# Kernel optimization log

Measured on AMD Instinct MI355X. Metric: run time of the kernel, lower is better.

The kernel has to match this reference:

```python
import jax, jax.numpy as jnp
import numpy as np

B, S, C = 4, 2048, 2048
D = C // 4  # head dim = 512

def setup_inputs() -> dict:
    key = jax.random.key(0)
    k1, k2, k3, k4, k5 = jax.random.split(key, 5)
    scale = 1.0 / np.sqrt(C)
    return {
        "x": jax.random.normal(k1, (B, S, C), dtype=jnp.float32),
        "Wqkv": jax.random.normal(k2, (3 * D, C), dtype=jnp.float32) * scale,
        "bqkv": jax.random.normal(k3, (3 * D,), dtype=jnp.float32) * 0.01,
        "Wo": jax.random.normal(k4, (C, D), dtype=jnp.float32) * (1.0 / np.sqrt(D)),
        "bo": jax.random.normal(k5, (C,), dtype=jnp.float32) * 0.01,
    }

def reference(x, Wqkv, bqkv, Wo, bo):
    Bx, Sx, Cx = x.shape
    d = Cx // 4
    # fused QKV projection: [B,S,3d] -> split into q,k,v each [B,S,d]
    qkv = jnp.einsum('bsc,oc->bso', x, Wqkv) + bqkv
    qkv = qkv.reshape(Bx, Sx, 3, d)
    q, k, v = qkv[:, :, 0], qkv[:, :, 1], qkv[:, :, 2]
    # scaled dot-product attention (full [B,S,S] scores, as in original)
    attn = jnp.einsum('bqd,bkd->bqk', q, k) / jnp.sqrt(jnp.asarray(d, x.dtype))
    attn = jax.nn.softmax(attn, axis=-1)
    ctx = jnp.einsum('bqk,bkd->bqd', attn, v)
    # output projection d -> C
    return jnp.einsum('bsd,od->bso', ctx, Wo) + bo
```

## Files before the change

kernel.cpp:

```cpp
#include <hip/hip_runtime.h>
#include <math.h>


typedef __bf16 bf16;
typedef bf16 bf16x8 __attribute__((ext_vector_type(8)));
typedef bf16 bf16x4 __attribute__((ext_vector_type(4)));
typedef float f32x4 __attribute__((ext_vector_type(4)));

#define BB 4
#define SS 2048
#define CC 2048
#define DD 512
#define ND3 1536
#define MM 8192

typedef const __attribute__((address_space(1))) unsigned int g_u32;
typedef __attribute__((address_space(3))) unsigned int l_u32;

__device__ __forceinline__ void gl_lds16(const bf16* g, bf16* l) {
    __builtin_amdgcn_global_load_lds((g_u32*)g, (l_u32*)l, 16, 0, 0);
}

#define N4_X   (MM * CC / 4)
#define N4_WQ  (ND3 * CC / 4)
#define N4_WO  (CC * DD / 4)
#define N4_RS  (MM / 4)
#define N4_TOT (N4_X + N4_WQ + N4_WO + N4_RS)

__global__ __launch_bounds__(256) void prep(const float* __restrict__ x,
                                            const float* __restrict__ Wqkv,
                                            const float* __restrict__ Wo,
                                            bf16* __restrict__ xb,
                                            bf16* __restrict__ wqkvb,
                                            bf16* __restrict__ wob,
                                            float* __restrict__ rsum) {
    int i = blockIdx.x * 256 + threadIdx.x;
    const int stride = gridDim.x * 256;
    for (; i < N4_TOT; i += stride) {
        if (i < N4_X + N4_WQ + N4_WO) {
            const float* src; bf16* dst; int j = i;
            if (j < N4_X)                { src = x;    dst = xb; }
            else if (j < N4_X + N4_WQ)   { src = Wqkv; dst = wqkvb; j -= N4_X; }
            else                         { src = Wo;   dst = wob;   j -= N4_X + N4_WQ; }
            float4 v = ((const float4*)src)[j];
            bf16x4 o;
            o[0] = (bf16)v.x; o[1] = (bf16)v.y; o[2] = (bf16)v.z; o[3] = (bf16)v.w;
            ((bf16x4*)dst)[j] = o;
        } else {
            int j = i - (N4_X + N4_WQ + N4_WO);
            ((float4*)rsum)[j] = float4{0.f, 0.f, 0.f, 0.f};
        }
    }
}

template <bool OUT_BF16, int BN, int EPI>
__global__ __launch_bounds__(256) void gemm_bt(const bf16* __restrict__ A,
                                               const bf16* __restrict__ Bm,
                                               const float* __restrict__ bias,
                                               float* __restrict__ rowsum,
                                               bf16* __restrict__ vTp,
                                               void* __restrict__ Cv,
                                               int K, int lda, int ldb, int ldc,
                                               long ab, long bb, long cb,
                                               float scale) {
    constexpr int TM = (BN == 128) ? 4 : 2;
    __shared__ bf16 As[128 * 32];
    __shared__ bf16 Bs[BN * 32];
    A += (size_t)blockIdx.z * ab;
    Bm += (size_t)blockIdx.z * bb;
    const int m0 = blockIdx.y * 128, n0 = blockIdx.x * BN;
    const int t = threadIdx.x, lane = t & 63, w = t >> 6;
    const int wm = (BN == 128) ? (w >> 1) * 64 : w * 32;
    const int wn = (BN == 128) ? (w & 1) * 64 : 0;
    const int q = lane >> 4, cl = lane & 15;
    const int srow = lane >> 2;
    const int scol = (lane & 3) * 8;
    const bf16* pa0 = A + (size_t)(m0 + w * 16 + srow) * lda + scol;
    const bf16* pa1 = pa0 + (size_t)64 * lda;
    const bf16* pb0 = Bm + (size_t)(n0 + w * 16 + srow) * ldb + scol;
    const bf16* pb1 = pb0 + (size_t)64 * ldb;
    bf16* lA0 = As + (w * 16) * 32;
    bf16* lA1 = As + (64 + w * 16) * 32;
    bf16* lB0 = Bs + (w * 16) * 32;
    bf16* lB1 = Bs + (64 + w * 16) * 32;

    f32x4 acc[TM][4] = {};
    for (int k0 = 0; k0 < K; k0 += 32) {
        gl_lds16(pa0 + k0, lA0);
        gl_lds16(pa1 + k0, lA1);
        gl_lds16(pb0 + k0, lB0);
        if constexpr (BN == 128) gl_lds16(pb1 + k0, lB1);
        __syncthreads();
        bf16x8 af[TM], bfr[4];
#pragma unroll
        for (int i = 0; i < TM; i++)
            af[i] = *(const bf16x8*)&As[(wm + i * 16 + cl) * 32 + q * 8];
#pragma unroll
        for (int j = 0; j < 4; j++)
            bfr[j] = *(const bf16x8*)&Bs[(wn + j * 16 + cl) * 32 + q * 8];
#pragma unroll
        for (int i = 0; i < TM; i++)
#pragma unroll
            for (int j = 0; j < 4; j++)
                acc[i][j] = __builtin_amdgcn_mfma_f32_16x16x32_bf16(af[i], bfr[j], acc[i][j], 0, 0, 0);
        __syncthreads();
    }

    const bool v_block = (EPI == 3) && (n0 >= 1024);
#pragma unroll
    for (int i = 0; i < TM; i++) {
        float inv[4];
        if constexpr (EPI == 2) {
#pragma unroll
            for (int r = 0; r < 4; r++)
                inv[r] = 1.0f / rowsum[(size_t)blockIdx.z * SS + m0 + wm + i * 16 + q * 4 + r];
        }
        float rp[4] = {0.f, 0.f, 0.f, 0.f};
#pragma unroll
        for (int j = 0; j < 4; j++) {
            int col = n0 + wn + j * 16 + cl;
            float bvv = ((EPI == 0 || EPI == 3) && bias) ? bias[col] : 0.0f;
            if (v_block) {
                int row = m0 + wm + i * 16 + q * 4;
                int b = row >> 11, s = row & 2047;
                bf16x4 o;
#pragma unroll
                for (int r = 0; r < 4; r++) o[r] = (bf16)(acc[i][j][r] * scale + bvv);
                *(bf16x4*)&vTp[((size_t)b * DD + (col - 1024)) * SS + s] = o;
            } else {
#pragma unroll
                for (int r = 0; r < 4; r++) {
                    int row = m0 + wm + i * 16 + q * 4 + r;
                    float val;
                    if constexpr (EPI == 1) { val = __expf(acc[i][j][r] * scale); rp[r] += val; }
                    else if constexpr (EPI == 2) { val = acc[i][j][r] * inv[r]; }
                    else { val = acc[i][j][r] * scale + bvv; }
                    if (OUT_BF16)
                        ((bf16*)Cv)[(size_t)blockIdx.z * cb + (size_t)row * ldc + col] = (bf16)val;
                    else
                        ((float*)Cv)[(size_t)blockIdx.z * cb + (size_t)row * ldc + col] = val;
                }
            }
        }
        if constexpr (EPI == 1) {
#pragma unroll
            for (int r = 0; r < 4; r++) {
#pragma unroll
                for (int off = 1; off < 16; off <<= 1)
                    rp[r] += __shfl_xor(rp[r], off, 64);
            }
            if (cl == 0) {
#pragma unroll
                for (int r = 0; r < 4; r++)
                    atomicAdd(&rowsum[(size_t)blockIdx.z * SS + m0 + wm + i * 16 + q * 4 + r], rp[r]);
            }
        }
    }
}

extern "C" void kernel_launch(void* const* d_in, const int* in_sizes, int n_in,
                              void* d_out, int out_size, void* d_ws, size_t ws_size,
                              hipStream_t stream) {
    const float* x    = (const float*)d_in[0];
    const float* Wqkv = (const float*)d_in[1];
    const float* bqkv = (const float*)d_in[2];
    const float* Wo   = (const float*)d_in[3];
    const float* bo   = (const float*)d_in[4];
    float* out = (float*)d_out;

    char* ws = (char*)d_ws;
    size_t off = 0;
    bf16* xb    = (bf16*)(ws + off); off += (size_t)MM * CC * 2;
    bf16* wqkvb = (bf16*)(ws + off); off += (size_t)ND3 * CC * 2;
    bf16* wob   = (bf16*)(ws + off); off += (size_t)CC * DD * 2;
    bf16* qkvb  = (bf16*)(ws + off); off += (size_t)MM * ND3 * 2;
    bf16* vT    = (bf16*)(ws + off); off += (size_t)BB * DD * SS * 2;
    bf16* expS  = (bf16*)(ws + off); off += (size_t)BB * SS * SS * 2;
    bf16* ctxb  = (bf16*)(ws + off); off += (size_t)MM * DD * 2;
    float* rsum = (float*)(ws + off); off += (size_t)MM * 4;

    prep<<<2048, 256, 0, stream>>>(x, Wqkv, Wo, xb, wqkvb, wob, rsum);

    gemm_bt<true, 128, 3><<<dim3(ND3 / 128, MM / 128, 1), 256, 0, stream>>>(
        xb, wqkvb, bqkv, nullptr, vT, qkvb, CC, CC, CC, ND3, 0, 0, 0, 1.0f);

    gemm_bt<true, 128, 1><<<dim3(SS / 128, SS / 128, BB), 256, 0, stream>>>(
        qkvb , qkvb + 512 , nullptr, rsum, nullptr, expS,
        DD, ND3, ND3, SS,
        (long)SS * ND3, (long)SS * ND3, (long)SS * SS,
        0.044194173824159216f );

    gemm_bt<true, 64, 2><<<dim3(DD / 64, SS / 128, BB), 256, 0, stream>>>(
        expS, vT, nullptr, rsum, nullptr, ctxb, SS, SS, SS, DD,
        (long)SS * SS, (long)DD * SS, (long)SS * DD, 1.0f);

    gemm_bt<false, 128, 0><<<dim3(CC / 128, MM / 128, 1), 256, 0, stream>>>(
        ctxb, wob, bo, nullptr, nullptr, out, DD, DD, DD, CC, 0, 0, 0, 1.0f);

    (void)in_sizes; (void)n_in; (void)out_size; (void)ws_size;
}
```

Before: 336.2 us.

## Compute attention GEMMs in transposed orientation with column-wise softmax sums

Swaps operand roles in the QK^T and PV GEMMs so each computes the transposed product (K·Q^T, then V^T·expS^T). New epilogues write bf16x4 vectors along the contiguous dimension instead of scalar strided stores, and sum exp values down columns with fewer shuffles. The PV kernel's grid is reoriented with 128-row tiles over head dim and 64-col tiles over queries. This targets the scalar bf16 store cost in the epilogues but changes the tile shape and the access pattern for the rowsum reads.

```diff
diff --git a/kernel.cpp b/kernel.cpp
--- a/kernel.cpp
+++ b/kernel.cpp
@@ -106,20 +106,55 @@
         __syncthreads();
     }
 
+    if constexpr (EPI == 4 || EPI == 5) {
+        float inv[4], cs[4] = {0.f, 0.f, 0.f, 0.f};
+        if constexpr (EPI == 5) {
+#pragma unroll
+            for (int j = 0; j < 4; j++)
+                inv[j] = 1.0f / rowsum[(size_t)blockIdx.z * SS + n0 + wn + j * 16 + cl];
+        }
+#pragma unroll
+        for (int i = 0; i < TM; i++)
+#pragma unroll
+            for (int j = 0; j < 4; j++) {
+                int col = n0 + wn + j * 16 + cl;
+                int row = m0 + wm + i * 16 + q * 4;
+                bf16x4 o;
+                if constexpr (EPI == 4) {
+#pragma unroll
+                    for (int r = 0; r < 4; r++) {
+                        float e = __expf(acc[i][j][r] * scale);
+                        cs[j] += e;
+                        o[r] = (bf16)e;
+                    }
+                } else {
+#pragma unroll
+                    for (int r = 0; r < 4; r++) o[r] = (bf16)(acc[i][j][r] * inv[j]);
+                }
+                *(bf16x4*)&((bf16*)Cv)[(size_t)blockIdx.z * cb + (size_t)col * ldc + row] = o;
+            }
+        if constexpr (EPI == 4) {
+#pragma unroll
+            for (int j = 0; j < 4; j++) {
+                cs[j] += __shfl_xor(cs[j], 16, 64);
+                cs[j] += __shfl_xor(cs[j], 32, 64);
+            }
+            if (q == 0) {
+#pragma unroll
+                for (int j = 0; j < 4; j++)
+                    atomicAdd(&rowsum[(size_t)blockIdx.z * SS + n0 + wn + j * 16 + cl], cs[j]);
+            }
+        }
+        return;
+    }
+
     const bool v_block = (EPI == 3) && (n0 >= 1024);
 #pragma unroll
     for (int i = 0; i < TM; i++) {
-        float inv[4];
-        if constexpr (EPI == 2) {
-#pragma unroll
-            for (int r = 0; r < 4; r++)
-                inv[r] = 1.0f / rowsum[(size_t)blockIdx.z * SS + m0 + wm + i * 16 + q * 4 + r];
-        }
-        float rp[4] = {0.f, 0.f, 0.f, 0.f};
 #pragma unroll
         for (int j = 0; j < 4; j++) {
             int col = n0 + wn + j * 16 + cl;
-            float bvv = ((EPI == 0 || EPI == 3) && bias) ? bias[col] : 0.0f;
+            float bvv = bias ? bias[col] : 0.0f;
             if (v_block) {
                 int row = m0 + wm + i * 16 + q * 4;
                 int b = row >> 11, s = row & 2047;
@@ -131,28 +166,12 @@
 #pragma unroll
                 for (int r = 0; r < 4; r++) {
                     int row = m0 + wm + i * 16 + q * 4 + r;
-                    float val;
-                    if constexpr (EPI == 1) { val = __expf(acc[i][j][r] * scale); rp[r] += val; }
-                    else if constexpr (EPI == 2) { val = acc[i][j][r] * inv[r]; }
-                    else { val = acc[i][j][r] * scale + bvv; }
+                    float val = acc[i][j][r] * scale + bvv;
                     if (OUT_BF16)
                         ((bf16*)Cv)[(size_t)blockIdx.z * cb + (size_t)row * ldc + col] = (bf16)val;
                     else
                         ((float*)Cv)[(size_t)blockIdx.z * cb + (size_t)row * ldc + col] = val;
                 }
-            }
-        }
-        if constexpr (EPI == 1) {
-#pragma unroll
-            for (int r = 0; r < 4; r++) {
-#pragma unroll
-                for (int off = 1; off < 16; off <<= 1)
-                    rp[r] += __shfl_xor(rp[r], off, 64);
-            }
-            if (cl == 0) {
-#pragma unroll
-                for (int r = 0; r < 4; r++)
-                    atomicAdd(&rowsum[(size_t)blockIdx.z * SS + m0 + wm + i * 16 + q * 4 + r], rp[r]);
             }
         }
     }
@@ -184,15 +203,16 @@
     gemm_bt<true, 128, 3><<<dim3(ND3 / 128, MM / 128, 1), 256, 0, stream>>>(
         xb, wqkvb, bqkv, nullptr, vT, qkvb, CC, CC, CC, ND3, 0, 0, 0, 1.0f);
 
-    gemm_bt<true, 128, 1><<<dim3(SS / 128, SS / 128, BB), 256, 0, stream>>>(
-        qkvb , qkvb + 512 , nullptr, rsum, nullptr, expS,
+    gemm_bt<true, 128, 4><<<dim3(SS / 128, SS / 128, BB), 256, 0, stream>>>(
+        qkvb + 512 , qkvb , nullptr, rsum, nullptr, expS,
         DD, ND3, ND3, SS,
         (long)SS * ND3, (long)SS * ND3, (long)SS * SS,
         0.044194173824159216f );
 
-    gemm_bt<true, 64, 2><<<dim3(DD / 64, SS / 128, BB), 256, 0, stream>>>(
-        expS, vT, nullptr, rsum, nullptr, ctxb, SS, SS, SS, DD,
-        (long)SS * SS, (long)DD * SS, (long)SS * DD, 1.0f);
+    gemm_bt<true, 64, 5><<<dim3(SS / 64, DD / 128, BB), 256, 0, stream>>>(
+        vT, expS, nullptr, rsum, nullptr, ctxb,
+        SS, SS, SS, DD,
+        (long)DD * SS, (long)SS * SS, (long)SS * DD, 1.0f);
 
     gemm_bt<false, 128, 0><<<dim3(CC / 128, MM / 128, 1), 256, 0, stream>>>(
         ctxb, wob, bo, nullptr, nullptr, out, DD, DD, DD, CC, 0, 0, 0, 1.0f);
```

After: 332.0 us. About the same (-1.3%).
